# Kernel tuning notes

Measured on AMD Instinct MI355X. Metric: run time of the kernel, lower is better.

Reference implementation:

```python
import jax, jax.numpy as jnp
import numpy as np

TEMP = 10.0  # config['attention_temperature']
N, F_IN, D = 8192, 129, 64  # items, n_features+1, attention_dim


def _mlp(x, W1, b1, W2, b2):
    # Linear -> ReLU -> Linear (has_skip_connection=False, has_batch_norm=False)
    h = jax.nn.relu(x @ W1 + b1)
    return h @ W2 + b2


def setup_inputs() -> dict:
    key = jax.random.key(0)
    ks = jax.random.split(key, 5)
    s1 = 1.0 / np.sqrt(F_IN)
    s2 = 1.0 / np.sqrt(D)
    return {
        "x": jax.random.normal(ks[0], (N, F_IN), dtype=jnp.float32),
        "Wq1": jax.random.normal(ks[1], (F_IN, D), dtype=jnp.float32) * s1,
        "bq1": jnp.zeros((D,), dtype=jnp.float32),
        "Wq2": jax.random.normal(ks[2], (D, D), dtype=jnp.float32) * s2,
        "bq2": jnp.zeros((D,), dtype=jnp.float32),
        "Wk1": jax.random.normal(ks[3], (F_IN, D), dtype=jnp.float32) * s1,
        "bk1": jnp.zeros((D,), dtype=jnp.float32),
        "Wk2": jax.random.normal(ks[4], (D, D), dtype=jnp.float32) * s2,
        "bk2": jnp.zeros((D,), dtype=jnp.float32),
    }


def reference(x, Wq1, bq1, Wq2, bq2, Wk1, bk1, Wk2, bk2):
    q = _mlp(x, Wq1, bq1, Wq2, bq2)          # [N, D]
    k = _mlp(x, Wk1, bk1, Wk2, bk2)          # [N, D]
    qkt = q @ k.T                             # [N, N]
    max_qkt = jnp.max(qkt, axis=-1)           # [N] row-max
    # torch broadcast: [N,N] / [N] divides column j by max of row j
    scaled = TEMP * qkt / max_qkt[None, :]
    return jax.nn.softmax(scaled, axis=-1)
```

## Files before the change

### kernel.cpp

```cpp
#include <hip/hip_runtime.h>
#include <math.h>

#define N 8192
#define FIN 129
#define D 64
#define TEMP 10.0f
#define LOG2E 1.4426950408889634f
#define SPLIT_S 32
#define SPLIT_W 32
#define RG 4
#define BROWS 256
#define MROWS 2

typedef _Float16 f16x8 __attribute__((ext_vector_type(8)));
typedef float    f32x4 __attribute__((ext_vector_type(4)));

#define MFMA16(A, B, C) __builtin_amdgcn_mfma_f32_16x16x32_f16((A), (B), (C), 0, 0, 0)

static __device__ inline float fast_exp2(float x) {
#if __has_builtin(__builtin_amdgcn_exp2f)
    return __builtin_amdgcn_exp2f(x);
#else
    float r; asm("v_exp_f32 %0, %1" : "=v"(r) : "v"(x)); return r;
#endif
}


__global__ __launch_bounds__(256) void k_mlp(
    const float* __restrict__ x,
    const float* __restrict__ Wq1, const float* __restrict__ bq1,
    const float* __restrict__ Wq2, const float* __restrict__ bq2,
    const float* __restrict__ Wk1, const float* __restrict__ bk1,
    const float* __restrict__ Wk2, const float* __restrict__ bk2,
    _Float16* __restrict__ qo, _Float16* __restrict__ ko)
{
    __shared__ float xs[4][MROWS][FIN];
    __shared__ float hqs[4][MROWS][D];
    __shared__ float hks[4][MROWS][D];
    const int wave  = threadIdx.x >> 6;
    const int lane  = threadIdx.x & 63;
    const int rbase = (blockIdx.x * 4 + wave) * MROWS;

    #pragma unroll
    for (int r = 0; r < MROWS; ++r) {
        const float* xr = x + (size_t)(rbase + r) * FIN;
        xs[wave][r][lane]      = xr[lane];
        xs[wave][r][64 + lane] = xr[64 + lane];
        if (lane == 0) xs[wave][r][128] = xr[128];
    }
    __syncthreads();

    float aq[MROWS], ak[MROWS];
    #pragma unroll
    for (int r = 0; r < MROWS; ++r) { aq[r] = bq1[lane]; ak[r] = bk1[lane]; }
    for (int f = 0; f < FIN; ++f) {
        const float wq = Wq1[f * D + lane];
        const float wk = Wk1[f * D + lane];
        #pragma unroll
        for (int r = 0; r < MROWS; ++r) {
            const float xv = xs[wave][r][f];
            aq[r] = fmaf(xv, wq, aq[r]);
            ak[r] = fmaf(xv, wk, ak[r]);
        }
    }
    #pragma unroll
    for (int r = 0; r < MROWS; ++r) {
        hqs[wave][r][lane] = fmaxf(aq[r], 0.f);
        hks[wave][r][lane] = fmaxf(ak[r], 0.f);
    }
    __syncthreads();

    float oq[MROWS], ok[MROWS];
    #pragma unroll
    for (int r = 0; r < MROWS; ++r) { oq[r] = bq2[lane]; ok[r] = bk2[lane]; }
    for (int t = 0; t < D; ++t) {
        const float wq2 = Wq2[t * D + lane];
        const float wk2 = Wk2[t * D + lane];
        #pragma unroll
        for (int r = 0; r < MROWS; ++r) {
            oq[r] = fmaf(hqs[wave][r][t], wq2, oq[r]);
            ok[r] = fmaf(hks[wave][r][t], wk2, ok[r]);
        }
    }
    #pragma unroll
    for (int r = 0; r < MROWS; ++r) {
        qo[(size_t)(rbase + r) * D + lane] = (_Float16)oq[r];
        ko[(size_t)(rbase + r) * D + lane] = (_Float16)ok[r];
    }
}

__global__ __launch_bounds__(256) void k_max(
    const _Float16* __restrict__ q16, const _Float16* __restrict__ k16,
    float* __restrict__ mpart)
{
    const int tid  = threadIdx.x;
    const int wave = tid >> 6;
    const int lane = tid & 63;
    const int lr   = lane & 15;
    const int lg   = lane >> 4;
    const int i0   = blockIdx.x * BROWS + wave * 64;
    const int jbase = blockIdx.y * (N / SPLIT_S);

    f16x8 b[RG][2];
    #pragma unroll
    for (int rg = 0; rg < RG; ++rg) {
        b[rg][0] = *reinterpret_cast<const f16x8*>(&q16[(i0 + rg * 16 + lr) * D + 8 * lg]);
        b[rg][1] = *reinterpret_cast<const f16x8*>(&q16[(i0 + rg * 16 + lr) * D + 32 + 8 * lg]);
    }

    float mx[RG];
    #pragma unroll
    for (int rg = 0; rg < RG; ++rg) mx[rg] = -INFINITY;

    f16x8 a0[4], a1[4];
    #pragma unroll
    for (int s = 0; s < 3; ++s) {
        const int jr = jbase + s * 16;
        a0[s] = *reinterpret_cast<const f16x8*>(&k16[(jr + lr) * D + 8 * lg]);
        a1[s] = *reinterpret_cast<const f16x8*>(&k16[(jr + lr) * D + 32 + 8 * lg]);
    }

    #pragma unroll
    for (int s = 0; s < 16; ++s) {
        if (s + 3 < 16) {
            const int jr = jbase + (s + 3) * 16;
            a0[(s + 3) & 3] = *reinterpret_cast<const f16x8*>(&k16[(jr + lr) * D + 8 * lg]);
            a1[(s + 3) & 3] = *reinterpret_cast<const f16x8*>(&k16[(jr + lr) * D + 32 + 8 * lg]);
        }
        #pragma unroll
        for (int rg = 0; rg < RG; ++rg) {
            f32x4 acc = {0.f, 0.f, 0.f, 0.f};
            acc = MFMA16(a0[s & 3], b[rg][0], acc);
            acc = MFMA16(a1[s & 3], b[rg][1], acc);
            mx[rg] = fmaxf(mx[rg], fmaxf(fmaxf(acc[0], acc[1]), fmaxf(acc[2], acc[3])));
        }
    }

    #pragma unroll
    for (int rg = 0; rg < RG; ++rg) {
        mx[rg] = fmaxf(mx[rg], __shfl_xor(mx[rg], 16));
        mx[rg] = fmaxf(mx[rg], __shfl_xor(mx[rg], 32));
    }
    if (lane < 16) {
        #pragma unroll
        for (int rg = 0; rg < RG; ++rg)
            mpart[blockIdx.y * N + i0 + rg * 16 + lr] = mx[rg];
    }
}

__global__ __launch_bounds__(256) void k_sumL(
    const _Float16* __restrict__ q16, const _Float16* __restrict__ k16,
    const float* __restrict__ mpart, float* __restrict__ Lpart)
{
    const int tid  = threadIdx.x;
    const int wave = tid >> 6;
    const int lane = tid & 63;
    const int lr   = lane & 15;
    const int lg   = lane >> 4;
    const int i0   = blockIdx.x * BROWS + wave * 64;
    const int jbase = blockIdx.y * (N / SPLIT_S);

    __shared__ float rinv_s[N / SPLIT_S];
    {
        float m = mpart[jbase + tid];
        #pragma unroll
        for (int s = 1; s < SPLIT_S; ++s) m = fmaxf(m, mpart[s * N + jbase + tid]);
        rinv_s[tid] = TEMP * LOG2E / m;
    }

    f16x8 b[RG][2];
    #pragma unroll
    for (int rg = 0; rg < RG; ++rg) {
        b[rg][0] = *reinterpret_cast<const f16x8*>(&q16[(i0 + rg * 16 + lr) * D + 8 * lg]);
        b[rg][1] = *reinterpret_cast<const f16x8*>(&q16[(i0 + rg * 16 + lr) * D + 32 + 8 * lg]);
    }
    __syncthreads();

    float sm[RG];
    #pragma unroll
    for (int rg = 0; rg < RG; ++rg) sm[rg] = 0.f;

    f16x8 a0[4], a1[4];
    #pragma unroll
    for (int s = 0; s < 3; ++s) {
        const int jr = jbase + s * 16;
        a0[s] = *reinterpret_cast<const f16x8*>(&k16[(jr + lr) * D + 8 * lg]);
        a1[s] = *reinterpret_cast<const f16x8*>(&k16[(jr + lr) * D + 32 + 8 * lg]);
    }

    #pragma unroll
    for (int s = 0; s < 16; ++s) {
        if (s + 3 < 16) {
            const int jr = jbase + (s + 3) * 16;
            a0[(s + 3) & 3] = *reinterpret_cast<const f16x8*>(&k16[(jr + lr) * D + 8 * lg]);
            a1[(s + 3) & 3] = *reinterpret_cast<const f16x8*>(&k16[(jr + lr) * D + 32 + 8 * lg]);
        }
        const float4 r4 = *reinterpret_cast<const float4*>(&rinv_s[s * 16 + lg * 4]);
        #pragma unroll
        for (int rg = 0; rg < RG; ++rg) {
            f32x4 acc = {0.f, 0.f, 0.f, 0.f};
            acc = MFMA16(a0[s & 3], b[rg][0], acc);
            acc = MFMA16(a1[s & 3], b[rg][1], acc);
            sm[rg] += fast_exp2(acc[0] * r4.x) + fast_exp2(acc[1] * r4.y)
                    + fast_exp2(acc[2] * r4.z) + fast_exp2(acc[3] * r4.w);
        }
    }

    #pragma unroll
    for (int rg = 0; rg < RG; ++rg) {
        sm[rg] += __shfl_xor(sm[rg], 16);
        sm[rg] += __shfl_xor(sm[rg], 32);
    }
    if (lane < 16) {
        #pragma unroll
        for (int rg = 0; rg < RG; ++rg)
            Lpart[blockIdx.y * N + i0 + rg * 16 + lr] = sm[rg];
    }
}

__global__ __launch_bounds__(256) void k_write(
    const _Float16* __restrict__ q16, const _Float16* __restrict__ k16,
    const float* __restrict__ mpart, const float* __restrict__ Lpart,
    float* __restrict__ out)
{
    const int tid  = threadIdx.x;
    const int wave = tid >> 6;
    const int lane = tid & 63;
    const int lr   = lane & 15;
    const int lg   = lane >> 4;
    const int i0b  = blockIdx.x * BROWS;
    const int i0   = i0b + wave * 64;
    const int jbase = blockIdx.y * (N / SPLIT_W);

    __shared__ float rinv_s[N / SPLIT_W];
    __shared__ float linv_s[BROWS];
    {
        float m = mpart[jbase + tid];
        #pragma unroll
        for (int s = 1; s < SPLIT_S; ++s) m = fmaxf(m, mpart[s * N + jbase + tid]);
        rinv_s[tid] = TEMP * LOG2E / m;
        float L = Lpart[i0b + tid];
        #pragma unroll
        for (int s = 1; s < SPLIT_S; ++s) L += Lpart[s * N + i0b + tid];
        linv_s[tid] = 1.f / L;
    }

    f16x8 b[RG][2];
    #pragma unroll
    for (int rg = 0; rg < RG; ++rg) {
        b[rg][0] = *reinterpret_cast<const f16x8*>(&q16[(i0 + rg * 16 + lr) * D + 8 * lg]);
        b[rg][1] = *reinterpret_cast<const f16x8*>(&q16[(i0 + rg * 16 + lr) * D + 32 + 8 * lg]);
    }
    __syncthreads();

    float Lvi[RG];
    #pragma unroll
    for (int rg = 0; rg < RG; ++rg) Lvi[rg] = linv_s[wave * 64 + rg * 16 + lr];

    f16x8 a[2][4];
    a[0][0] = *reinterpret_cast<const f16x8*>(&k16[(jbase + lr) * D + 8 * lg]);
    a[0][1] = *reinterpret_cast<const f16x8*>(&k16[(jbase + lr) * D + 32 + 8 * lg]);
    a[0][2] = *reinterpret_cast<const f16x8*>(&k16[(jbase + 16 + lr) * D + 8 * lg]);
    a[0][3] = *reinterpret_cast<const f16x8*>(&k16[(jbase + 16 + lr) * D + 32 + 8 * lg]);

    #pragma unroll
    for (int s2 = 0; s2 < 8; ++s2) {
        const int p = s2 & 1;
        if (s2 + 1 < 8) {
            const int jn = jbase + (s2 + 1) * 32;
            a[1 - p][0] = *reinterpret_cast<const f16x8*>(&k16[(jn + lr) * D + 8 * lg]);
            a[1 - p][1] = *reinterpret_cast<const f16x8*>(&k16[(jn + lr) * D + 32 + 8 * lg]);
            a[1 - p][2] = *reinterpret_cast<const f16x8*>(&k16[(jn + 16 + lr) * D + 8 * lg]);
            a[1 - p][3] = *reinterpret_cast<const f16x8*>(&k16[(jn + 16 + lr) * D + 32 + 8 * lg]);
        }
        const int j0 = jbase + s2 * 32;
        const float4 r40 = *reinterpret_cast<const float4*>(&rinv_s[s2 * 32 + lg * 4]);
        const float4 r41 = *reinterpret_cast<const float4*>(&rinv_s[s2 * 32 + 16 + lg * 4]);
        #pragma unroll
        for (int rg = 0; rg < RG; ++rg) {
            f32x4 acc0 = {0.f, 0.f, 0.f, 0.f};
            acc0 = MFMA16(a[p][0], b[rg][0], acc0);
            acc0 = MFMA16(a[p][1], b[rg][1], acc0);
            f32x4 acc1 = {0.f, 0.f, 0.f, 0.f};
            acc1 = MFMA16(a[p][2], b[rg][0], acc1);
            acc1 = MFMA16(a[p][3], b[rg][1], acc1);
            float4 o0, o1;
            o0.x = fast_exp2(acc0[0] * r40.x) * Lvi[rg];
            o0.y = fast_exp2(acc0[1] * r40.y) * Lvi[rg];
            o0.z = fast_exp2(acc0[2] * r40.z) * Lvi[rg];
            o0.w = fast_exp2(acc0[3] * r40.w) * Lvi[rg];
            o1.x = fast_exp2(acc1[0] * r41.x) * Lvi[rg];
            o1.y = fast_exp2(acc1[1] * r41.y) * Lvi[rg];
            o1.z = fast_exp2(acc1[2] * r41.z) * Lvi[rg];
            o1.w = fast_exp2(acc1[3] * r41.w) * Lvi[rg];
            float* rowp = out + (size_t)(i0 + rg * 16 + lr) * N + j0;
            *reinterpret_cast<float4*>(rowp + lg * 4)      = o0;
            *reinterpret_cast<float4*>(rowp + 16 + lg * 4) = o1;
        }
    }
}

extern "C" void kernel_launch(void* const* d_in, const int* in_sizes, int n_in,
                              void* d_out, int out_size, void* d_ws, size_t ws_size,
                              hipStream_t stream)
{
    const float* x   = (const float*)d_in[0];
    const float* Wq1 = (const float*)d_in[1];
    const float* bq1 = (const float*)d_in[2];
    const float* Wq2 = (const float*)d_in[3];
    const float* bq2 = (const float*)d_in[4];
    const float* Wk1 = (const float*)d_in[5];
    const float* bk1 = (const float*)d_in[6];
    const float* Wk2 = (const float*)d_in[7];
    const float* bk2 = (const float*)d_in[8];

    float* out = (float*)d_out;

    _Float16* q16 = (_Float16*)d_ws;
    _Float16* k16 = q16 + (size_t)N * D;
    float* mpart  = (float*)(k16 + (size_t)N * D);
    float* Lpart  = mpart + (size_t)SPLIT_S * N;

    k_mlp  <<<N / (4 * MROWS), 256, 0, stream>>>(x, Wq1, bq1, Wq2, bq2, Wk1, bk1, Wk2, bk2, q16, k16);
    k_max  <<<dim3(N / BROWS, SPLIT_S), 256, 0, stream>>>(q16, k16, mpart);
    k_sumL <<<dim3(N / BROWS, SPLIT_S), 256, 0, stream>>>(q16, k16, mpart, Lpart);
    k_write<<<dim3(N / BROWS, SPLIT_W), 256, 0, stream>>>(q16, k16, mpart, Lpart, out);
}
```

Measured before the change: 117.5 us.

## Compute MLP on MFMA with split-fp16 hi/lo emulation of fp32

```diff
diff --git a/kernel.cpp b/kernel.cpp
--- a/kernel.cpp
+++ b/kernel.cpp
@@ -4,15 +4,16 @@
 #define N 8192
 #define FIN 129
 #define D 64
+#define KP 160
 #define TEMP 10.0f
 #define LOG2E 1.4426950408889634f
 #define SPLIT_S 32
 #define SPLIT_W 32
 #define RG 4
 #define BROWS 256
-#define MROWS 2
 
 typedef _Float16 f16x8 __attribute__((ext_vector_type(8)));
+typedef _Float16 f16x4 __attribute__((ext_vector_type(4)));
 typedef float    f32x4 __attribute__((ext_vector_type(4)));
 
 #define MFMA16(A, B, C) __builtin_amdgcn_mfma_f32_16x16x32_f16((A), (B), (C), 0, 0, 0)
@@ -26,66 +27,132 @@
 }
 
 
-__global__ __launch_bounds__(256) void k_mlp(
-    const float* __restrict__ x,
-    const float* __restrict__ Wq1, const float* __restrict__ bq1,
-    const float* __restrict__ Wq2, const float* __restrict__ bq2,
-    const float* __restrict__ Wk1, const float* __restrict__ bk1,
-    const float* __restrict__ Wk2, const float* __restrict__ bk2,
+__global__ __launch_bounds__(256) void k_prep_x(
+    const float* __restrict__ x, _Float16* __restrict__ xhi, _Float16* __restrict__ xlo)
+{
+    const int wave = threadIdx.x >> 6, lane = threadIdx.x & 63;
+    const int r = blockIdx.x * 4 + wave;
+    #pragma unroll
+    for (int c0 = 0; c0 < KP; c0 += 64) {
+        const int c = c0 + lane;
+        if (c < KP) {
+            const float v = (c < FIN) ? x[(size_t)r * FIN + c] : 0.f;
+            const _Float16 h = (_Float16)v;
+            xhi[(size_t)r * KP + c] = h;
+            xlo[(size_t)r * KP + c] = (_Float16)(v - (float)h);
+        }
+    }
+}
+
+__global__ __launch_bounds__(256) void k_prep_w(
+    const float* __restrict__ Wq1, const float* __restrict__ Wk1,
+    const float* __restrict__ Wq2, const float* __restrict__ Wk2,
+    _Float16* __restrict__ w1thi, _Float16* __restrict__ w1tlo,
+    _Float16* __restrict__ w2thi, _Float16* __restrict__ w2tlo)
+{
+    for (int idx = threadIdx.x; idx < 2 * 64 * KP; idx += 256) {
+        const int side = idx / (64 * KP);
+        const int rem  = idx % (64 * KP);
+        const int d = rem / KP, f = rem % KP;
+        const float* W = side ? Wk1 : Wq1;
+        const float v = (f < FIN) ? W[f * 64 + d] : 0.f;
+        const _Float16 h = (_Float16)v;
+        w1thi[idx] = h;
+        w1tlo[idx] = (_Float16)(v - (float)h);
+    }
+    for (int idx = threadIdx.x; idx < 2 * 64 * 64; idx += 256) {
+        const int side = idx / 4096;
+        const int rem  = idx % 4096;
+        const int d = rem / 64, t = rem % 64;
+        const float* W = side ? Wk2 : Wq2;
+        const float v = W[t * 64 + d];
+        const _Float16 h = (_Float16)v;
+        w2thi[idx] = h;
+        w2tlo[idx] = (_Float16)(v - (float)h);
+    }
+}
+
+__global__ __launch_bounds__(64) void k_mlp2(
+    const _Float16* __restrict__ xhi, const _Float16* __restrict__ xlo,
+    const _Float16* __restrict__ w1thi, const _Float16* __restrict__ w1tlo,
+    const _Float16* __restrict__ w2thi, const _Float16* __restrict__ w2tlo,
+    const float* __restrict__ bq1, const float* __restrict__ bk1,
+    const float* __restrict__ bq2, const float* __restrict__ bk2,
     _Float16* __restrict__ qo, _Float16* __restrict__ ko)
 {
-    __shared__ float xs[4][MROWS][FIN];
-    __shared__ float hqs[4][MROWS][D];
-    __shared__ float hks[4][MROWS][D];
-    const int wave  = threadIdx.x >> 6;
-    const int lane  = threadIdx.x & 63;
-    const int rbase = (blockIdx.x * 4 + wave) * MROWS;
-
-    #pragma unroll
-    for (int r = 0; r < MROWS; ++r) {
-        const float* xr = x + (size_t)(rbase + r) * FIN;
-        xs[wave][r][lane]      = xr[lane];
-        xs[wave][r][64 + lane] = xr[64 + lane];
-        if (lane == 0) xs[wave][r][128] = xr[128];
+    const int lane = threadIdx.x & 63;
+    const int lr = lane & 15, lg = lane >> 4;
+    const int r0 = blockIdx.x * 16;
+    const int side = blockIdx.y;
+
+    const _Float16* W1h = w1thi + side * (64 * KP);
+    const _Float16* W1l = w1tlo + side * (64 * KP);
+    const _Float16* W2h = w2thi + side * (64 * 64);
+    const _Float16* W2l = w2tlo + side * (64 * 64);
+    const float* b1 = side ? bk1 : bq1;
+    const float* b2 = side ? bk2 : bq2;
+    _Float16* out = side ? ko : qo;
+
+    __shared__ _Float16 hh[16][80];
+    __shared__ _Float16 hl[16][80];
+
+    f16x8 bh[5], bl[5];
+    #pragma unroll
+    for (int kf = 0; kf < 5; ++kf) {
+        bh[kf] = *reinterpret_cast<const f16x8*>(&xhi[(size_t)(r0 + lr) * KP + kf * 32 + 8 * lg]);
+        bl[kf] = *reinterpret_cast<const f16x8*>(&xlo[(size_t)(r0 + lr) * KP + kf * 32 + 8 * lg]);
+    }
+
+    #pragma unroll
+    for (int rf = 0; rf < 4; ++rf) {
+        f32x4 acc = {0.f, 0.f, 0.f, 0.f};
+        #pragma unroll
+        for (int kf = 0; kf < 5; ++kf) {
+            const f16x8 ah = *reinterpret_cast<const f16x8*>(&W1h[(rf * 16 + lr) * KP + kf * 32 + 8 * lg]);
+            const f16x8 al = *reinterpret_cast<const f16x8*>(&W1l[(rf * 16 + lr) * KP + kf * 32 + 8 * lg]);
+            acc = MFMA16(al, bh[kf], acc);
+            acc = MFMA16(ah, bl[kf], acc);
+            acc = MFMA16(ah, bh[kf], acc);
+        }
+        const float4 bb = *reinterpret_cast<const float4*>(&b1[rf * 16 + lg * 4]);
+        const float h0 = fmaxf(acc[0] + bb.x, 0.f);
+        const float h1 = fmaxf(acc[1] + bb.y, 0.f);
+        const float h2 = fmaxf(acc[2] + bb.z, 0.f);
+        const float h3 = fmaxf(acc[3] + bb.w, 0.f);
+        f16x4 vh, vl;
+        vh[0] = (_Float16)h0; vl[0] = (_Float16)(h0 - (float)vh[0]);
+        vh[1] = (_Float16)h1; vl[1] = (_Float16)(h1 - (float)vh[1]);
+        vh[2] = (_Float16)h2; vl[2] = (_Float16)(h2 - (float)vh[2]);
+        vh[3] = (_Float16)h3; vl[3] = (_Float16)(h3 - (float)vh[3]);
+        *reinterpret_cast<f16x4*>(&hh[lr][rf * 16 + lg * 4]) = vh;
+        *reinterpret_cast<f16x4*>(&hl[lr][rf * 16 + lg * 4]) = vl;
     }
     __syncthreads();
 
-    float aq[MROWS], ak[MROWS];
-    #pragma unroll
-    for (int r = 0; r < MROWS; ++r) { aq[r] = bq1[lane]; ak[r] = bk1[lane]; }
-    for (int f = 0; f < FIN; ++f) {
-        const float wq = Wq1[f * D + lane];
-        const float wk = Wk1[f * D + lane];
-        #pragma unroll
-        for (int r = 0; r < MROWS; ++r) {
-            const float xv = xs[wave][r][f];
-            aq[r] = fmaf(xv, wq, aq[r]);
-            ak[r] = fmaf(xv, wk, ak[r]);
-        }
-    }
-    #pragma unroll
-    for (int r = 0; r < MROWS; ++r) {
-        hqs[wave][r][lane] = fmaxf(aq[r], 0.f);
-        hks[wave][r][lane] = fmaxf(ak[r], 0.f);
-    }
-    __syncthreads();
-
-    float oq[MROWS], ok[MROWS];
-    #pragma unroll
-    for (int r = 0; r < MROWS; ++r) { oq[r] = bq2[lane]; ok[r] = bk2[lane]; }
-    for (int t = 0; t < D; ++t) {
-        const float wq2 = Wq2[t * D + lane];
-        const float wk2 = Wk2[t * D + lane];
-        #pragma unroll
-        for (int r = 0; r < MROWS; ++r) {
-            oq[r] = fmaf(hqs[wave][r][t], wq2, oq[r]);
-            ok[r] = fmaf(hks[wave][r][t], wk2, ok[r]);
-        }
-    }
-    #pragma unroll
-    for (int r = 0; r < MROWS; ++r) {
-        qo[(size_t)(rbase + r) * D + lane] = (_Float16)oq[r];
-        ko[(size_t)(rbase + r) * D + lane] = (_Float16)ok[r];
+    f16x8 b2h[2], b2l[2];
+    #pragma unroll
+    for (int kf = 0; kf < 2; ++kf) {
+        b2h[kf] = *reinterpret_cast<const f16x8*>(&hh[lr][kf * 32 + 8 * lg]);
+        b2l[kf] = *reinterpret_cast<const f16x8*>(&hl[lr][kf * 32 + 8 * lg]);
+    }
+    #pragma unroll
+    for (int rf = 0; rf < 4; ++rf) {
+        f32x4 acc = {0.f, 0.f, 0.f, 0.f};
+        #pragma unroll
+        for (int kf = 0; kf < 2; ++kf) {
+            const f16x8 ah = *reinterpret_cast<const f16x8*>(&W2h[(rf * 16 + lr) * 64 + kf * 32 + 8 * lg]);
+            const f16x8 al = *reinterpret_cast<const f16x8*>(&W2l[(rf * 16 + lr) * 64 + kf * 32 + 8 * lg]);
+            acc = MFMA16(al, b2h[kf], acc);
+            acc = MFMA16(ah, b2l[kf], acc);
+            acc = MFMA16(ah, b2h[kf], acc);
+        }
+        const float4 bb = *reinterpret_cast<const float4*>(&b2[rf * 16 + lg * 4]);
+        f16x4 o;
+        o[0] = (_Float16)(acc[0] + bb.x);
+        o[1] = (_Float16)(acc[1] + bb.y);
+        o[2] = (_Float16)(acc[2] + bb.z);
+        o[3] = (_Float16)(acc[3] + bb.w);
+        *reinterpret_cast<f16x4*>(&out[(size_t)(r0 + lr) * 64 + rf * 16 + lg * 4]) = o;
     }
 }
 
@@ -316,13 +383,22 @@
 
     float* out = (float*)d_out;
 
-    _Float16* q16 = (_Float16*)d_ws;
-    _Float16* k16 = q16 + (size_t)N * D;
-    float* mpart  = (float*)(k16 + (size_t)N * D);
-    float* Lpart  = mpart + (size_t)SPLIT_S * N;
-
-    k_mlp  <<<N / (4 * MROWS), 256, 0, stream>>>(x, Wq1, bq1, Wq2, bq2, Wk1, bk1, Wk2, bk2, q16, k16);
-    k_max  <<<dim3(N / BROWS, SPLIT_S), 256, 0, stream>>>(q16, k16, mpart);
-    k_sumL <<<dim3(N / BROWS, SPLIT_S), 256, 0, stream>>>(q16, k16, mpart, Lpart);
-    k_write<<<dim3(N / BROWS, SPLIT_W), 256, 0, stream>>>(q16, k16, mpart, Lpart, out);
-}
+    _Float16* q16   = (_Float16*)d_ws;
+    _Float16* k16   = q16 + (size_t)N * D;
+    _Float16* xhi   = k16 + (size_t)N * D;
+    _Float16* xlo   = xhi + (size_t)N * KP;
+    _Float16* w1thi = xlo + (size_t)N * KP;
+    _Float16* w1tlo = w1thi + 2 * 64 * KP;
+    _Float16* w2thi = w1tlo + 2 * 64 * KP;
+    _Float16* w2tlo = w2thi + 2 * 64 * 64;
+    float* mpart = (float*)(w2tlo + 2 * 64 * 64);
+    float* Lpart = mpart + (size_t)SPLIT_S * N;
+
+    k_prep_x<<<N / 4, 256, 0, stream>>>(x, xhi, xlo);
+    k_prep_w<<<1, 256, 0, stream>>>(Wq1, Wk1, Wq2, Wk2, w1thi, w1tlo, w2thi, w2tlo);
+    k_mlp2  <<<dim3(N / 16, 2), 64, 0, stream>>>(xhi, xlo, w1thi, w1tlo, w2thi, w2tlo,
+                                                 bq1, bk1, bq2, bk2, q16, k16);
+    k_max   <<<dim3(N / BROWS, SPLIT_S), 256, 0, stream>>>(q16, k16, mpart);
+    k_sumL  <<<dim3(N / BROWS, SPLIT_S), 256, 0, stream>>>(q16, k16, mpart, Lpart);
+    k_write <<<dim3(N / BROWS, SPLIT_W), 256, 0, stream>>>(q16, k16, mpart, Lpart, out);
+}
```

New measurement: 136.2 us. 16.0% more time.
